# Optimization experiments

Measured on AMD Instinct MI355X. Metric: run time of the kernel, lower is better.

The kernel has to match this reference:

```python
import jax, jax.numpy as jnp
import numpy as np
import math

H = 512       # hidden_dim
NL = 4        # num_layers
N2 = 32       # d_state // 2
B, L = 8, 4096
DT_MIN, DT_MAX = 1e-3, 1e-1
EPS = 1e-5


def _layer_norm(x, gamma, beta):
    mu = jnp.mean(x, axis=-1, keepdims=True)
    var = jnp.mean(jnp.square(x - mu), axis=-1, keepdims=True)
    return (x - mu) * jax.lax.rsqrt(var + EPS) * gamma + beta


def setup_inputs() -> dict:
    key = jax.random.key(0)
    ks = jax.random.split(key, 8)
    x = jax.random.normal(ks[0], (B, L, H), dtype=jnp.float32)
    # S4DKernel buffers / params, stacked over layers
    log_dt = jax.random.uniform(ks[1], (NL, H)) * (math.log(DT_MAX) - math.log(DT_MIN)) + math.log(DT_MIN)
    A_imag = jnp.broadcast_to(math.pi * jnp.arange(N2, dtype=jnp.float32), (NL, H, N2)).copy()
    log_A_real = jnp.full((NL, H, N2), math.log(0.5), dtype=jnp.float32)
    C = jax.random.normal(ks[2], (NL, H, N2, 2), dtype=jnp.float32)  # view_as_real of cfloat
    D = jax.random.normal(ks[3], (NL, H), dtype=jnp.float32)
    # 1x1 Conv1d h -> 2h (pointwise linear over channels)
    W = jax.random.normal(ks[4], (NL, 2 * H, H), dtype=jnp.float32) / math.sqrt(H)
    b = jax.random.normal(ks[5], (NL, 2 * H), dtype=jnp.float32) * 0.01
    gamma = jnp.ones((NL, H), dtype=jnp.float32)
    beta = jnp.zeros((NL, H), dtype=jnp.float32)
    return dict(x=x, log_dt=log_dt, A_imag=A_imag, log_A_real=log_A_real,
                C=C, D=D, W=W, b=b, gamma=gamma, beta=beta)


def reference(x, log_dt, A_imag, log_A_real, C, D, W, b, gamma, beta):
    Bsz, Lseq, h = x.shape
    t = jnp.arange(Lseq, dtype=jnp.float32)
    for i in range(NL):
        # --- S4D kernel generation ---
        dt = jnp.exp(log_dt[i])                                    # (h,)
        Cc = C[i, ..., 0] + 1j * C[i, ..., 1]                      # (h, n)
        A = -jnp.exp(log_A_real[i]) + 1j * A_imag[i]               # (h, n)
        dA = A * dt[:, None]                                       # (h, n)
        Cmod = Cc * (jnp.exp(dA) - 1.0) / A                        # (h, n)
        # Vandermonde: exp(dA * l), reduced over state dim
        K = 2.0 * jnp.einsum('hn,hnl->hl', Cmod,
                             jnp.exp(dA[:, :, None] * t)).real     # (h, L)
        # --- FFT long convolution ---
        u = jnp.transpose(x, (0, 2, 1))                            # (B, h, L)
        kf = jnp.fft.rfft(K, n=2 * Lseq)                           # (h, L+1)
        uf = jnp.fft.rfft(u, n=2 * Lseq)                           # (B, h, L+1)
        y = jnp.fft.irfft(uf * kf, n=2 * Lseq)[..., :Lseq]         # (B, h, L)
        y = y + u * D[i][:, None]
        y = jax.nn.gelu(y, approximate=False)                      # torch nn.GELU default (erf)
        # 1x1 conv h -> 2h then GLU over channel dim
        z = jnp.einsum('oh,bhl->bol', W[i], y) + b[i][None, :, None]
        a, g = jnp.split(z, 2, axis=1)
        y = a * jax.nn.sigmoid(g)                                  # (B, h, L)
        y = jnp.transpose(y, (0, 2, 1))                            # (B, L, h)
        x = _layer_norm(y + x, gamma[i], beta[i])
    return x
```

## Files before the change

kernel.cpp:

```cpp
#include <hip/hip_runtime.h>
#include <hip/hip_bf16.h>
#include <math.h>

#define H 512
#define NL 4
#define N2 32
#define Bsz 8
#define Lseq 4096
#define BT (Bsz*Lseq)
#define LC2 64
#define NCC (BT/LC2)
#define CPB (Lseq/LC2)

typedef __attribute__((ext_vector_type(8))) short short8;
typedef __attribute__((ext_vector_type(4))) float float4v;


__device__ __forceinline__ float bf2f(unsigned short u) {
    union { unsigned int i; float f; } x; x.i = ((unsigned int)u) << 16; return x.f;
}
__device__ __forceinline__ unsigned short f2bf(float f) {
    union { float f; unsigned int i; } x; x.f = f;
    unsigned int u = x.i + 0x7fff + ((x.i >> 16) & 1);
    return (unsigned short)(u >> 16);
}
__device__ __forceinline__ uint2 pack4bf(float a, float b, float c, float d) {
    uint2 r;
    r.x = (unsigned)f2bf(a) | ((unsigned)f2bf(b) << 16);
    r.y = (unsigned)f2bf(c) | ((unsigned)f2bf(d) << 16);
    return r;
}
__device__ __forceinline__ void async_copy16(const void* g, void* l) {
    __builtin_amdgcn_global_load_lds(
        (const __attribute__((address_space(1))) void*)g,
        (__attribute__((address_space(3))) void*)l, 16, 0, 0);
}

__global__ void wconv_kernel(const float* __restrict__ W, unsigned short* __restrict__ Wbf) {
    int tid = blockIdx.x * 256 + threadIdx.x;
    Wbf[tid] = f2bf(W[tid]);
}

__global__ void params_kernel(const float* __restrict__ log_dt, const float* __restrict__ A_imag,
                              const float* __restrict__ log_A_real, const float* __restrict__ Cin,
                              float* __restrict__ dA, float* __restrict__ Ct) {
    int tid = blockIdx.x * 256 + threadIdx.x;
    int h = tid % H;
    int n = (tid / H) % N2;
    int layer = tid / (H * N2);
    float dt = expf(log_dt[layer * H + h]);
    int pidx = (layer * H + h) * N2 + n;
    float Are = -expf(log_A_real[pidx]);
    float Aim = A_imag[pidx];
    float dre = Are * dt, dim = Aim * dt;
    float er = expf(dre);
    float lre = er * cosf(dim), lim = er * sinf(dim);
    float nre = lre - 1.0f, nim = lim;
    float inv = 1.0f / (Are * Are + Aim * Aim);
    float tre = (nre * Are + nim * Aim) * inv;
    float tim = (nim * Are - nre * Aim) * inv;
    float Ccre = Cin[pidx * 2], Ccim = Cin[pidx * 2 + 1];
    int oidx = ((layer * N2 + n) * 2) * H + h;
    dA[oidx] = dre;  dA[oidx + H] = dim;
    Ct[oidx] = 2.0f * (Ccre * tre - Ccim * tim);
    Ct[oidx + H] = 2.0f * (Ccre * tim + Ccim * tre);
}

__global__ void kergen_k_kernel(const float* __restrict__ dA, const float* __restrict__ Ct,
                                unsigned short* __restrict__ kmat) {
    int t = blockIdx.x * 256 + threadIdx.x;
    int d = t & 63;
    int h = (t >> 6) & (H - 1);
    int layer = t >> 15;
    float fd = (float)d;
    float sum = 0.f;
    for (int n = 0; n < N2; n++) {
        int base = ((layer * N2 + n) * 2) * H + h;
        float dre = dA[base], dim = dA[base + H];
        float Ctr = Ct[base], Cti = Ct[base + H];
        float e = expf(dre * fd);
        sum += Ctr * e * cosf(dim * fd) - Cti * e * sinf(dim * fd);
    }
    kmat[t] = f2bf(sum);
}

__global__ void kergenW_kernel(const float* __restrict__ dA, unsigned short* __restrict__ Wst, int layer) {
    int t = blockIdx.x * 256 + threadIdx.x;
    int j = t & 63;
    int r = (t >> 6) & 63;
    int h = t >> 12;
    int n = r >> 1;
    int base = ((layer * N2 + n) * 2) * H + h;
    float dre = dA[base], dim = dA[base + H];
    float p = (float)(63 - j);
    float e = expf(dre * p);
    Wst[t] = f2bf((r & 1) ? e * sinf(dim * p) : e * cosf(dim * p));
}

__global__ void kergenV_kernel(const float* __restrict__ dA, const float* __restrict__ Ct,
                               unsigned short* __restrict__ Vl, int layer) {
    int t = blockIdx.x * 256 + threadIdx.x;
    int c2 = t & 63;
    int l = (t >> 6) & 63;
    int h = t >> 12;
    int n = c2 >> 1;
    int base = ((layer * N2 + n) * 2) * H + h;
    float dre = dA[base], dim = dA[base + H];
    float Ctr = Ct[base], Cti = Ct[base + H];
    float q = (float)(l + 1);
    float e = expf(dre * q);
    float ar = e * cosf(dim * q), ai = e * sinf(dim * q);
    float vre = Ctr * ar - Cti * ai;
    float vim = Ctr * ai + Cti * ar;
    Vl[t] = f2bf((c2 & 1) ? -vim : vre);
}

__global__ __launch_bounds__(256) void transpose1_kernel(const float* __restrict__ xi,
                                                         unsigned short* __restrict__ ut) {
    __shared__ float tile[64][68];
    int bx = blockIdx.x;
    int pt = bx & 511, ht = bx >> 9;
    int p0 = pt * 64, h0 = ht * 64;
    int t = threadIdx.x;
    int jr = t & 15, ib = t >> 4;
#pragma unroll
    for (int pass = 0; pass < 4; pass++) {
        int i = ib + pass * 16;
        float4 v = *(const float4*)(xi + (size_t)(p0 + i) * H + h0 + jr * 4);
        tile[i][jr * 4 + 0] = v.x; tile[i][jr * 4 + 1] = v.y;
        tile[i][jr * 4 + 2] = v.z; tile[i][jr * 4 + 3] = v.w;
    }
    __syncthreads();
#pragma unroll
    for (int pass = 0; pass < 4; pass++) {
        int i2 = ib + pass * 16;
        int j2 = jr * 4;
        uint2 pk = pack4bf(tile[j2][i2], tile[j2 + 1][i2], tile[j2 + 2][i2], tile[j2 + 3][i2]);
        *(uint2*)(ut + (size_t)(h0 + i2) * BT + p0 + j2) = pk;
    }
}

__global__ __launch_bounds__(256) void states_kernel(const unsigned short* __restrict__ ut,
                                                     const unsigned short* __restrict__ Wst,
                                                     unsigned short* __restrict__ Sloc) {
    int h = blockIdx.x;
    int wave = threadIdx.x >> 6, lane = threadIdx.x & 63;
    int r16 = lane & 15, quad = lane >> 4;
    const unsigned short* uh = ut + (size_t)h * BT;
    const unsigned short* wh = Wst + (size_t)h * 64 * 64;
    unsigned short* sh = Sloc + (size_t)h * NCC * 64;
    for (int nt = 0; nt < 8; nt++) {
        int cc0 = wave * 128 + nt * 16;
        float4v acc[4] = {};
#pragma unroll
        for (int k0 = 0; k0 < 64; k0 += 32) {
            short8 bf = *reinterpret_cast<const short8*>(uh + (size_t)(cc0 + r16) * 64 + k0 + quad * 8);
#pragma unroll
            for (int mt = 0; mt < 4; mt++) {
                short8 af = *reinterpret_cast<const short8*>(wh + (mt * 16 + r16) * 64 + k0 + quad * 8);
                acc[mt] = __builtin_amdgcn_mfma_f32_16x16x32_bf16(af, bf, acc[mt], 0, 0, 0);
            }
        }
        int cc = cc0 + r16;
#pragma unroll
        for (int mt = 0; mt < 4; mt++) {
            uint2 pk = pack4bf(acc[mt][0], acc[mt][1], acc[mt][2], acc[mt][3]);
            *(uint2*)(sh + (size_t)cc * 64 + mt * 16 + quad * 4) = pk;
        }
    }
}

__global__ void combine_kernel(unsigned short* __restrict__ Sloc, const float* __restrict__ dA, int layer) {
    int t = blockIdx.x * 256 + threadIdx.x;
    int n = t & 31;
    int b = (t >> 5) & 7;
    int h = t >> 8;
    int base = ((layer * N2 + n) * 2) * H + h;
    float dre = dA[base], dim = dA[base + H];
    float e = expf(dre * 64.f);
    float Lr = e * cosf(dim * 64.f), Li = e * sinf(dim * 64.f);
    unsigned int* p = (unsigned int*)Sloc + ((size_t)h * NCC + b * CPB) * 32 + n;
    float sr = 0.f, si = 0.f;
    for (int c = 0; c < CPB; c++) {
        unsigned int v = p[(size_t)c * 32];
        float pr = bf2f(v & 0xffff), pi = bf2f(v >> 16);
        p[(size_t)c * 32] = (unsigned)f2bf(sr) | ((unsigned)f2bf(si) << 16);
        float nr = fmaf(Lr, sr, fmaf(-Li, si, pr));
        float ni = fmaf(Lr, si, fmaf(Li, sr, pi));
        sr = nr; si = ni;
    }
}

__global__ __launch_bounds__(256) void conv_kernel(const unsigned short* __restrict__ ut,
                                                   const unsigned short* __restrict__ kmat,
                                                   const unsigned short* __restrict__ Vl,
                                                   const unsigned short* __restrict__ Sent,
                                                   const float* __restrict__ Dp,
                                                   unsigned short* __restrict__ yt, int layer) {
    __shared__ unsigned short T[64][72];
    int h = blockIdx.x, half = blockIdx.y;
    int t = threadIdx.x;
    const unsigned short* km = kmat + ((size_t)layer * H + h) * 64;
    {
        int l = t >> 2, j0 = (t & 3) * 16;
#pragma unroll
        for (int g = 0; g < 2; g++) {
            short8 v;
#pragma unroll
            for (int e = 0; e < 8; e++) {
                int j = j0 + g * 8 + e;
                v[e] = (j <= l) ? (short)km[l - j] : (short)0;
            }
            *reinterpret_cast<short8*>(&T[l][j0 + g * 8]) = v;
        }
    }
    __syncthreads();
    int wave = t >> 6, lane = t & 63;
    int r16 = lane & 15, quad = lane >> 4;
    const unsigned short* uh = ut + (size_t)h * BT;
    const unsigned short* vh = Vl + (size_t)h * 64 * 64;
    const unsigned short* eh = Sent + (size_t)h * NCC * 64;
    unsigned short* yh = yt + (size_t)h * BT;
    float Dh = Dp[layer * H + h];
    for (int nt = 0; nt < 4; nt++) {
        int cc0 = half * 256 + wave * 64 + nt * 16;
        float4v acc[4] = {};
#pragma unroll
        for (int k0 = 0; k0 < 64; k0 += 32) {
            short8 bf = *reinterpret_cast<const short8*>(uh + (size_t)(cc0 + r16) * 64 + k0 + quad * 8);
#pragma unroll
            for (int mt = 0; mt < 4; mt++) {
                short8 af = *reinterpret_cast<const short8*>(&T[mt * 16 + r16][k0 + quad * 8]);
                acc[mt] = __builtin_amdgcn_mfma_f32_16x16x32_bf16(af, bf, acc[mt], 0, 0, 0);
            }
        }
#pragma unroll
        for (int k0 = 0; k0 < 64; k0 += 32) {
            short8 bf = *reinterpret_cast<const short8*>(eh + (size_t)(cc0 + r16) * 64 + k0 + quad * 8);
#pragma unroll
            for (int mt = 0; mt < 4; mt++) {
                short8 af = *reinterpret_cast<const short8*>(vh + (mt * 16 + r16) * 64 + k0 + quad * 8);
                acc[mt] = __builtin_amdgcn_mfma_f32_16x16x32_bf16(af, bf, acc[mt], 0, 0, 0);
            }
        }
        int cc = cc0 + r16;
#pragma unroll
        for (int mt = 0; mt < 4; mt++) {
            size_t p = (size_t)cc * 64 + mt * 16 + quad * 4;
            ushort4 uu = *(const ushort4*)(uh + p);
            float o[4];
#pragma unroll
            for (int r = 0; r < 4; r++) {
                float y = acc[mt][r] + Dh * bf2f(((const unsigned short*)&uu)[r]);
                o[r] = 0.5f * y * (1.0f + erff(y * 0.70710678118654752f));
            }
            *(uint2*)(yh + p) = pack4bf(o[0], o[1], o[2], o[3]);
        }
    }
}

__global__ __launch_bounds__(256) void transpose2_kernel(const unsigned short* __restrict__ yt,
                                                         unsigned short* __restrict__ yb) {
    __shared__ unsigned short tile[64][72];
    int bx = blockIdx.x;
    int pt = bx & 511, ht = bx >> 9;
    int p0 = pt * 64, h0 = ht * 64;
    int t = threadIdx.x;
    int jr = t & 7, ib = t >> 3;
#pragma unroll
    for (int pass = 0; pass < 2; pass++) {
        int i = ib + pass * 32;
        short8 v = *reinterpret_cast<const short8*>(yt + (size_t)(h0 + i) * BT + p0 + jr * 8);
#pragma unroll
        for (int e = 0; e < 8; e++) tile[i][jr * 8 + e] = (unsigned short)v[e];
    }
    __syncthreads();
    int pp = t >> 2, hg = t & 3;
    short8 o0, o1;
#pragma unroll
    for (int r = 0; r < 8; r++) o0[r] = (short)tile[hg * 16 + r][pp];
#pragma unroll
    for (int r = 0; r < 8; r++) o1[r] = (short)tile[hg * 16 + 8 + r][pp];
    unsigned short* dst = yb + (size_t)(p0 + pp) * H + h0 + hg * 16;
    *reinterpret_cast<short8*>(dst) = o0;
    *reinterpret_cast<short8*>(dst + 8) = o1;
}

__global__ __launch_bounds__(256) void gemm_glu_kernel(const unsigned short* __restrict__ ybf,
                                                       const unsigned short* __restrict__ Wbf,
                                                       const float* __restrict__ bias,
                                                       unsigned short* __restrict__ yo, int layer) {
    __shared__ unsigned short As[128 * 32];
    __shared__ unsigned short Bs[128 * 32];
    int tid = threadIdx.x;
    int wave = tid >> 6, lane = tid & 63;
    int wr = wave >> 1, wc = wave & 1;
    int r16 = lane & 15, quad = lane >> 4;
    int m0 = blockIdx.x * 128;
    int o0 = blockIdx.y * 64;
    const unsigned short* Wl = Wbf + (size_t)layer * 2 * H * H;

    int srow = lane >> 2;
    int scol = (lane & 3) * 8;
    const unsigned short* aSrc0 = ybf + ((size_t)(m0 + wave * 16 + srow)) * H + scol;
    const unsigned short* aSrc1 = aSrc0 + (size_t)64 * H;
    const unsigned short* bSrcA = Wl + ((size_t)(o0 + wave * 16 + srow)) * H + scol;
    const unsigned short* bSrcG = bSrcA + (size_t)512 * H;
    unsigned short* aDst0 = As + (wave * 16) * 32;
    unsigned short* aDst1 = As + (64 + wave * 16) * 32;
    unsigned short* bDstA = Bs + (wave * 16) * 32;
    unsigned short* bDstG = Bs + (64 + wave * 16) * 32;

    float4v acc_a[4][2] = {}, acc_g[4][2] = {};

    for (int k0 = 0; k0 < H; k0 += 32) {
        __syncthreads();
        async_copy16(aSrc0, aDst0);
        async_copy16(aSrc1, aDst1);
        async_copy16(bSrcA, bDstA);
        async_copy16(bSrcG, bDstG);
        aSrc0 += 32; aSrc1 += 32; bSrcA += 32; bSrcG += 32;
        __syncthreads();

        short8 af[4], ba[2], bg[2];
#pragma unroll
        for (int mi = 0; mi < 4; mi++)
            af[mi] = *reinterpret_cast<const short8*>(As + (wr * 64 + mi * 16 + r16) * 32 + quad * 8);
#pragma unroll
        for (int ni = 0; ni < 2; ni++) {
            ba[ni] = *reinterpret_cast<const short8*>(Bs + (wc * 32 + ni * 16 + r16) * 32 + quad * 8);
            bg[ni] = *reinterpret_cast<const short8*>(Bs + (64 + wc * 32 + ni * 16 + r16) * 32 + quad * 8);
        }
#pragma unroll
        for (int mi = 0; mi < 4; mi++)
#pragma unroll
            for (int ni = 0; ni < 2; ni++) {
                acc_a[mi][ni] = __builtin_amdgcn_mfma_f32_16x16x32_bf16(af[mi], ba[ni], acc_a[mi][ni], 0, 0, 0);
                acc_g[mi][ni] = __builtin_amdgcn_mfma_f32_16x16x32_bf16(af[mi], bg[ni], acc_g[mi][ni], 0, 0, 0);
            }
    }

    const float* bl = bias + layer * 2 * H;
#pragma unroll
    for (int ni = 0; ni < 2; ni++) {
        int o = o0 + wc * 32 + ni * 16 + r16;
        float ba_ = bl[o], bg_ = bl[H + o];
#pragma unroll
        for (int mi = 0; mi < 4; mi++)
#pragma unroll
            for (int r = 0; r < 4; r++) {
                int l = m0 + wr * 64 + mi * 16 + quad * 4 + r;
                float av = acc_a[mi][ni][r] + ba_;
                float gv = acc_g[mi][ni][r] + bg_;
                yo[(size_t)l * H + o] = f2bf(av * (1.0f / (1.0f + expf(-gv))));
            }
    }
}

__global__ __launch_bounds__(256) void ln_kernel(const unsigned short* __restrict__ yo,
                                                 const float* __restrict__ xin,
                                                 const float* __restrict__ gamma, const float* __restrict__ beta,
                                                 float* __restrict__ xout, int layer) {
    int wave = threadIdx.x >> 6, lane = threadIdx.x & 63;
    size_t row = (size_t)blockIdx.x * 4 + wave;
    const unsigned short* yp = yo + row * H + lane * 8;
    const float* xp = xin + row * H + lane * 8;
    short8 yv = *reinterpret_cast<const short8*>(yp);
    float4 x0 = *(const float4*)(xp);
    float4 x1 = *(const float4*)(xp + 4);
    float v[8];
    v[0] = bf2f((unsigned short)yv[0]) + x0.x; v[1] = bf2f((unsigned short)yv[1]) + x0.y;
    v[2] = bf2f((unsigned short)yv[2]) + x0.z; v[3] = bf2f((unsigned short)yv[3]) + x0.w;
    v[4] = bf2f((unsigned short)yv[4]) + x1.x; v[5] = bf2f((unsigned short)yv[5]) + x1.y;
    v[6] = bf2f((unsigned short)yv[6]) + x1.z; v[7] = bf2f((unsigned short)yv[7]) + x1.w;
    float s = 0.f, s2 = 0.f;
#pragma unroll
    for (int i = 0; i < 8; i++) { s += v[i]; s2 = fmaf(v[i], v[i], s2); }
#pragma unroll
    for (int off = 32; off; off >>= 1) {
        s += __shfl_xor(s, off);
        s2 += __shfl_xor(s2, off);
    }
    float mu = s * (1.0f / H);
    float var = s2 * (1.0f / H) - mu * mu;
    float inv = rsqrtf(var + 1e-5f);
    const float* gl = gamma + layer * H + lane * 8;
    const float* bl = beta + layer * H + lane * 8;
    float* op = xout + row * H + lane * 8;
#pragma unroll
    for (int i = 0; i < 8; i++)
        op[i] = (v[i] - mu) * inv * gl[i] + bl[i];
}

extern "C" void kernel_launch(void* const* d_in, const int* in_sizes, int n_in,
                              void* d_out, int out_size, void* d_ws, size_t ws_size,
                              hipStream_t stream) {
    const float* x          = (const float*)d_in[0];
    const float* log_dt     = (const float*)d_in[1];
    const float* A_imag     = (const float*)d_in[2];
    const float* log_A_real = (const float*)d_in[3];
    const float* C          = (const float*)d_in[4];
    const float* D          = (const float*)d_in[5];
    const float* W          = (const float*)d_in[6];
    const float* bias       = (const float*)d_in[7];
    const float* gamma      = (const float*)d_in[8];
    const float* beta       = (const float*)d_in[9];

    char* ws = (char*)d_ws;
    float*          xA   = (float*)(ws + 0);
    unsigned short* Sloc = (unsigned short*)(ws + 67108864);
    unsigned short* u_t  = (unsigned short*)(ws + 100663296);
    unsigned short* ybf  = (unsigned short*)(ws + 100663296);
    unsigned short* y_t  = (unsigned short*)(ws + 134217728);
    unsigned short* yo   = (unsigned short*)(ws + 134217728);
    unsigned short* Wbf  = (unsigned short*)(ws + 167772160);
    unsigned short* WV   = (unsigned short*)(ws + 171966464);
    unsigned short* kmat = (unsigned short*)(ws + 176160768);
    float*          dA   = (float*)(ws + 176422912);
    float*          Ct   = (float*)(ws + 176947200);
    float* xout_final    = (float*)d_out;

    wconv_kernel<<<NL * 2 * H * H / 256, 256, 0, stream>>>(W, Wbf);
    params_kernel<<<NL * N2 * H / 256, 256, 0, stream>>>(log_dt, A_imag, log_A_real, C, dA, Ct);
    kergen_k_kernel<<<NL * H * 64 / 256, 256, 0, stream>>>(dA, Ct, kmat);

    const float* xi = x;
    float* bufs[NL] = { xA, xout_final, xA, xout_final };
    for (int layer = 0; layer < NL; ++layer) {
        float* xo = bufs[layer];
        transpose1_kernel<<<4096, 256, 0, stream>>>(xi, u_t);
        kergenW_kernel<<<H * 64 * 64 / 256, 256, 0, stream>>>(dA, WV, layer);
        states_kernel<<<H, 256, 0, stream>>>(u_t, WV, Sloc);
        combine_kernel<<<H * Bsz * N2 / 256, 256, 0, stream>>>(Sloc, dA, layer);
        kergenV_kernel<<<H * 64 * 64 / 256, 256, 0, stream>>>(dA, Ct, WV, layer);
        conv_kernel<<<dim3(H, 2), 256, 0, stream>>>(u_t, kmat, WV, Sloc, D, y_t, layer);
        transpose2_kernel<<<4096, 256, 0, stream>>>(y_t, ybf);
        gemm_glu_kernel<<<dim3(BT / 128, H / 64), 256, 0, stream>>>(ybf, Wbf, bias, yo, layer);
        ln_kernel<<<BT / 4, 256, 0, stream>>>(yo, xi, gamma, beta, xo, layer);
        xi = xo;
    }
}
```

Before: 923.0 us.

## Store inter-layer residual in bf16 and swizzle GEMM shared-memory columns

The residual stream between layers is now kept in bf16 instead of fp32. A new bf16 transpose kernel and a bf16 path in the layernorm kernel cut the global memory traffic of the transpose and layernorm kernels, and the layernorm stores are vectorized. The GLU GEMM also XOR-swizzles its shared-memory column index on both write and read to reduce LDS bank conflicts. The cost is extra rounding of the residual at every layer boundary, which may reduce accuracy.

```diff
diff --git a/kernel.cpp b/kernel.cpp
--- a/kernel.cpp
+++ b/kernel.cpp
@@ -115,8 +115,8 @@
     Vl[t] = f2bf((c2 & 1) ? -vim : vre);
 }
 
-__global__ __launch_bounds__(256) void transpose1_kernel(const float* __restrict__ xi,
-                                                         unsigned short* __restrict__ ut) {
+__global__ __launch_bounds__(256) void t1_f32_kernel(const float* __restrict__ xi,
+                                                     unsigned short* __restrict__ ut) {
     __shared__ float tile[64][68];
     int bx = blockIdx.x;
     int pt = bx & 511, ht = bx >> 9;
@@ -138,6 +138,33 @@
         uint2 pk = pack4bf(tile[j2][i2], tile[j2 + 1][i2], tile[j2 + 2][i2], tile[j2 + 3][i2]);
         *(uint2*)(ut + (size_t)(h0 + i2) * BT + p0 + j2) = pk;
     }
+}
+
+__global__ __launch_bounds__(256) void t1_bf16_kernel(const unsigned short* __restrict__ xi,
+                                                      unsigned short* __restrict__ ut) {
+    __shared__ unsigned short tile[64][72];
+    int bx = blockIdx.x;
+    int pt = bx & 511, ht = bx >> 9;
+    int p0 = pt * 64, h0 = ht * 64;
+    int t = threadIdx.x;
+    int jr = t & 7, ib = t >> 3;
+#pragma unroll
+    for (int pass = 0; pass < 2; pass++) {
+        int i = ib + pass * 32;
+        short8 v = *reinterpret_cast<const short8*>(xi + (size_t)(p0 + i) * H + h0 + jr * 8);
+#pragma unroll
+        for (int e = 0; e < 8; e++) tile[i][jr * 8 + e] = (unsigned short)v[e];
+    }
+    __syncthreads();
+    int hr = t >> 2, bg = t & 3;
+    short8 o0, o1;
+#pragma unroll
+    for (int r = 0; r < 8; r++) o0[r] = (short)tile[bg * 16 + r][hr];
+#pragma unroll
+    for (int r = 0; r < 8; r++) o1[r] = (short)tile[bg * 16 + 8 + r][hr];
+    unsigned short* dst = ut + (size_t)(h0 + hr) * BT + p0 + bg * 16;
+    *reinterpret_cast<short8*>(dst) = o0;
+    *reinterpret_cast<short8*>(dst + 8) = o1;
 }
 
 __global__ __launch_bounds__(256) void states_kernel(const unsigned short* __restrict__ ut,
@@ -301,7 +328,7 @@
     const unsigned short* Wl = Wbf + (size_t)layer * 2 * H * H;
 
     int srow = lane >> 2;
-    int scol = (lane & 3) * 8;
+    int scol = ((lane & 3) ^ ((srow >> 1) & 3)) * 8;
     const unsigned short* aSrc0 = ybf + ((size_t)(m0 + wave * 16 + srow)) * H + scol;
     const unsigned short* aSrc1 = aSrc0 + (size_t)64 * H;
     const unsigned short* bSrcA = Wl + ((size_t)(o0 + wave * 16 + srow)) * H + scol;
@@ -311,6 +338,8 @@
     unsigned short* bDstA = Bs + (wave * 16) * 32;
     unsigned short* bDstG = Bs + (64 + wave * 16) * 32;
 
+    int rcol = (quad ^ ((r16 >> 1) & 3)) * 8;
+
     float4v acc_a[4][2] = {}, acc_g[4][2] = {};
 
     for (int k0 = 0; k0 < H; k0 += 32) {
@@ -325,11 +354,11 @@
         short8 af[4], ba[2], bg[2];
 #pragma unroll
         for (int mi = 0; mi < 4; mi++)
-            af[mi] = *reinterpret_cast<const short8*>(As + (wr * 64 + mi * 16 + r16) * 32 + quad * 8);
+            af[mi] = *reinterpret_cast<const short8*>(As + (wr * 64 + mi * 16 + r16) * 32 + rcol);
 #pragma unroll
         for (int ni = 0; ni < 2; ni++) {
-            ba[ni] = *reinterpret_cast<const short8*>(Bs + (wc * 32 + ni * 16 + r16) * 32 + quad * 8);
-            bg[ni] = *reinterpret_cast<const short8*>(Bs + (64 + wc * 32 + ni * 16 + r16) * 32 + quad * 8);
+            ba[ni] = *reinterpret_cast<const short8*>(Bs + (wc * 32 + ni * 16 + r16) * 32 + rcol);
+            bg[ni] = *reinterpret_cast<const short8*>(Bs + (64 + wc * 32 + ni * 16 + r16) * 32 + rcol);
         }
 #pragma unroll
         for (int mi = 0; mi < 4; mi++)
@@ -358,21 +387,31 @@
 }
 
 __global__ __launch_bounds__(256) void ln_kernel(const unsigned short* __restrict__ yo,
-                                                 const float* __restrict__ xin,
+                                                 const float* __restrict__ xf,
+                                                 const unsigned short* __restrict__ xb,
                                                  const float* __restrict__ gamma, const float* __restrict__ beta,
-                                                 float* __restrict__ xout, int layer) {
+                                                 float* __restrict__ of, unsigned short* __restrict__ ob,
+                                                 int in_f32, int out_f32, int layer) {
     int wave = threadIdx.x >> 6, lane = threadIdx.x & 63;
     size_t row = (size_t)blockIdx.x * 4 + wave;
     const unsigned short* yp = yo + row * H + lane * 8;
-    const float* xp = xin + row * H + lane * 8;
     short8 yv = *reinterpret_cast<const short8*>(yp);
-    float4 x0 = *(const float4*)(xp);
-    float4 x1 = *(const float4*)(xp + 4);
     float v[8];
-    v[0] = bf2f((unsigned short)yv[0]) + x0.x; v[1] = bf2f((unsigned short)yv[1]) + x0.y;
-    v[2] = bf2f((unsigned short)yv[2]) + x0.z; v[3] = bf2f((unsigned short)yv[3]) + x0.w;
-    v[4] = bf2f((unsigned short)yv[4]) + x1.x; v[5] = bf2f((unsigned short)yv[5]) + x1.y;
-    v[6] = bf2f((unsigned short)yv[6]) + x1.z; v[7] = bf2f((unsigned short)yv[7]) + x1.w;
+    if (in_f32) {
+        const float* xp = xf + row * H + lane * 8;
+        float4 x0 = *(const float4*)(xp);
+        float4 x1 = *(const float4*)(xp + 4);
+        v[0] = bf2f((unsigned short)yv[0]) + x0.x; v[1] = bf2f((unsigned short)yv[1]) + x0.y;
+        v[2] = bf2f((unsigned short)yv[2]) + x0.z; v[3] = bf2f((unsigned short)yv[3]) + x0.w;
+        v[4] = bf2f((unsigned short)yv[4]) + x1.x; v[5] = bf2f((unsigned short)yv[5]) + x1.y;
+        v[6] = bf2f((unsigned short)yv[6]) + x1.z; v[7] = bf2f((unsigned short)yv[7]) + x1.w;
+    } else {
+        const unsigned short* xp = xb + row * H + lane * 8;
+        short8 xv = *reinterpret_cast<const short8*>(xp);
+#pragma unroll
+        for (int i = 0; i < 8; i++)
+            v[i] = bf2f((unsigned short)yv[i]) + bf2f((unsigned short)xv[i]);
+    }
     float s = 0.f, s2 = 0.f;
 #pragma unroll
     for (int i = 0; i < 8; i++) { s += v[i]; s2 = fmaf(v[i], v[i], s2); }
@@ -386,10 +425,21 @@
     float inv = rsqrtf(var + 1e-5f);
     const float* gl = gamma + layer * H + lane * 8;
     const float* bl = beta + layer * H + lane * 8;
-    float* op = xout + row * H + lane * 8;
+    float o[8];
 #pragma unroll
     for (int i = 0; i < 8; i++)
-        op[i] = (v[i] - mu) * inv * gl[i] + bl[i];
+        o[i] = (v[i] - mu) * inv * gl[i] + bl[i];
+    if (out_f32) {
+        float* op = of + row * H + lane * 8;
+        *(float4*)(op) = make_float4(o[0], o[1], o[2], o[3]);
+        *(float4*)(op + 4) = make_float4(o[4], o[5], o[6], o[7]);
+    } else {
+        unsigned short* op = ob + row * H + lane * 8;
+        uint2 p0 = pack4bf(o[0], o[1], o[2], o[3]);
+        uint2 p1 = pack4bf(o[4], o[5], o[6], o[7]);
+        *(uint2*)(op) = p0;
+        *(uint2*)(op + 4) = p1;
+    }
 }
 
 extern "C" void kernel_launch(void* const* d_in, const int* in_sizes, int n_in,
@@ -407,7 +457,7 @@
     const float* beta       = (const float*)d_in[9];
 
     char* ws = (char*)d_ws;
-    float*          xA   = (float*)(ws + 0);
+    unsigned short* xR   = (unsigned short*)(ws + 0);
     unsigned short* Sloc = (unsigned short*)(ws + 67108864);
     unsigned short* u_t  = (unsigned short*)(ws + 100663296);
     unsigned short* ybf  = (unsigned short*)(ws + 100663296);
@@ -424,11 +474,11 @@
     params_kernel<<<NL * N2 * H / 256, 256, 0, stream>>>(log_dt, A_imag, log_A_real, C, dA, Ct);
     kergen_k_kernel<<<NL * H * 64 / 256, 256, 0, stream>>>(dA, Ct, kmat);
 
-    const float* xi = x;
-    float* bufs[NL] = { xA, xout_final, xA, xout_final };
     for (int layer = 0; layer < NL; ++layer) {
-        float* xo = bufs[layer];
-        transpose1_kernel<<<4096, 256, 0, stream>>>(xi, u_t);
+        if (layer == 0)
+            t1_f32_kernel<<<4096, 256, 0, stream>>>(x, u_t);
+        else
+            t1_bf16_kernel<<<4096, 256, 0, stream>>>(xR, u_t);
         kergenW_kernel<<<H * 64 * 64 / 256, 256, 0, stream>>>(dA, WV, layer);
         states_kernel<<<H, 256, 0, stream>>>(u_t, WV, Sloc);
         combine_kernel<<<H * Bsz * N2 / 256, 256, 0, stream>>>(Sloc, dA, layer);
@@ -436,7 +486,8 @@
         conv_kernel<<<dim3(H, 2), 256, 0, stream>>>(u_t, kmat, WV, Sloc, D, y_t, layer);
         transpose2_kernel<<<4096, 256, 0, stream>>>(y_t, ybf);
         gemm_glu_kernel<<<dim3(BT / 128, H / 64), 256, 0, stream>>>(ybf, Wbf, bias, yo, layer);
-        ln_kernel<<<BT / 4, 256, 0, stream>>>(yo, xi, gamma, beta, xo, layer);
-        xi = xo;
-    }
-}
+        int in_f32 = (layer == 0), out_f32 = (layer == NL - 1);
+        ln_kernel<<<BT / 4, 256, 0, stream>>>(yo, x, xR, gamma, beta,
+                                              xout_final, xR, in_f32, out_f32, layer);
+    }
+}
```

Result: faster. 863.4 us (-6.5%).
